# Kernel optimization log

Measured on AMD Instinct MI355X. Metric: run time of the kernel, lower is better.

The kernel has to match this reference:

```python
import jax, jax.numpy as jnp
import numpy as np

NUM_GRAPHS = 512

def _add_self_loops(edge_index, n):
    loop = jnp.arange(n, dtype=edge_index.dtype)
    row = jnp.concatenate([edge_index[0], loop])
    col = jnp.concatenate([edge_index[1], loop])
    return row, col

def _gcn_conv(x, W, b, row, col, norm, n):
    h = x @ W                              # [N, H] dense transform
    msgs = h[row] * norm[:, None]          # gather + normalize, [E+N, H]
    out = jax.ops.segment_sum(msgs, col, num_segments=n)
    return out + b

def setup_inputs() -> dict:
    key = jax.random.key(0)
    ks = jax.random.split(key, 10)
    N, E, F_IN, H, C = 50000, 800000, 128, 128, 16
    s = 1.0 / np.sqrt(H)
    return {
        "x": jax.random.normal(ks[0], (N, F_IN), dtype=jnp.float32),
        "edge_index": jax.random.randint(ks[1], (2, E), 0, N, dtype=jnp.int64),
        "batch": jnp.sort(jax.random.randint(ks[2], (N,), 0, NUM_GRAPHS, dtype=jnp.int64)),
        "W1": jax.random.normal(ks[3], (F_IN, H), dtype=jnp.float32) * s,
        "b1": jnp.zeros((H,), dtype=jnp.float32),
        "W2": jax.random.normal(ks[4], (H, H), dtype=jnp.float32) * s,
        "b2": jnp.zeros((H,), dtype=jnp.float32),
        "W3": jax.random.normal(ks[5], (H, H), dtype=jnp.float32) * s,
        "b3": jnp.zeros((H,), dtype=jnp.float32),
        "lin_W": jax.random.normal(ks[6], (H, C), dtype=jnp.float32) * s,
        "lin_b": jnp.zeros((C,), dtype=jnp.float32),
    }

def reference(x, edge_index, batch, W1, b1, W2, b2, W3, b3, lin_W, lin_b):
    n = x.shape[0]
    row, col = _add_self_loops(edge_index, n)
    # symmetric degree normalization (computed once, shared by all layers)
    deg = jax.ops.segment_sum(jnp.ones_like(col, dtype=x.dtype), col, num_segments=n)
    dinv = jnp.where(deg > 0, jax.lax.rsqrt(deg), 0.0)
    norm = dinv[row] * dinv[col]           # [E+N]

    h = jax.nn.relu(_gcn_conv(x, W1, b1, row, col, norm, n))
    h = jax.nn.relu(_gcn_conv(h, W2, b2, row, col, norm, n))
    h = _gcn_conv(h, W3, b3, row, col, norm, n)

    # global mean pool over graphs in the batch
    pooled = jax.ops.segment_sum(h, batch, num_segments=NUM_GRAPHS)
    cnt = jax.ops.segment_sum(jnp.ones((n,), dtype=h.dtype), batch, num_segments=NUM_GRAPHS)
    pooled = pooled / jnp.maximum(cnt, 1.0)[:, None]

    # dropout is identity in eval mode
    return pooled @ lin_W + lin_b          # [NUM_GRAPHS, C]
```

## Files before the change

kernel.cpp:

```cpp
#include <hip/hip_runtime.h>
#include <hip/hip_bf16.h>

#define FEAT 128
#define NGRAPH 512
#define NCLS 16

typedef __attribute__((ext_vector_type(8))) short bf16x8;
typedef __attribute__((ext_vector_type(4))) float f32x4;


__device__ inline unsigned short f2bf(float f) {
    __hip_bfloat16 h = __float2bfloat16(f);
    return *(unsigned short*)&h;
}
__device__ inline float bf2f(unsigned short u) {
    return __uint_as_float((unsigned int)u << 16);
}
__device__ inline void unpk2(unsigned int u, float& lo, float& hi) {
    lo = __uint_as_float(u << 16);
    hi = __uint_as_float(u & 0xffff0000u);
}


__global__ void k_hist(const int* __restrict__ col, int* __restrict__ hist, int E) {
    int i = blockIdx.x * blockDim.x + threadIdx.x;
    if (i < E) atomicAdd(&hist[col[i]], 1);
}

__global__ void k_dinv(const int* __restrict__ hist, float* __restrict__ dinv, int N) {
    int i = blockIdx.x * blockDim.x + threadIdx.x;
    if (i < N) dinv[i] = rsqrtf((float)(hist[i] + 1));
}

__global__ void k_scanA(const int* __restrict__ hist, int* __restrict__ partial, int N) {
    __shared__ int s[256];
    int i = blockIdx.x * 256 + threadIdx.x;
    s[threadIdx.x] = (i < N) ? hist[i] : 0;
    __syncthreads();
    for (int off = 128; off > 0; off >>= 1) {
        if (threadIdx.x < off) s[threadIdx.x] += s[threadIdx.x + off];
        __syncthreads();
    }
    if (threadIdx.x == 0) partial[blockIdx.x] = s[0];
}

__global__ void k_scanB(int* __restrict__ partial, int nb) {
    __shared__ int s[256];
    int t = threadIdx.x;
    int orig = (t < nb) ? partial[t] : 0;
    s[t] = orig;
    __syncthreads();
    for (int off = 1; off < 256; off <<= 1) {
        int v = (t >= off) ? s[t - off] : 0;
        __syncthreads();
        s[t] += v;
        __syncthreads();
    }
    if (t < nb) partial[t] = s[t] - orig;
}

__global__ void k_scanC(const int* __restrict__ hist, const int* __restrict__ partial,
                        int* __restrict__ start, int* __restrict__ cur, int N) {
    __shared__ int s[256];
    int t = threadIdx.x;
    int i = blockIdx.x * 256 + t;
    int orig = (i < N) ? hist[i] : 0;
    s[t] = orig;
    __syncthreads();
    for (int off = 1; off < 256; off <<= 1) {
        int v = (t >= off) ? s[t - off] : 0;
        __syncthreads();
        s[t] += v;
        __syncthreads();
    }
    if (i < N) {
        int ex = s[t] - orig + partial[blockIdx.x];
        start[i] = ex;
        cur[i] = ex;
    }
}

__global__ void k_fill(const int* __restrict__ row, const int* __restrict__ col,
                       int* __restrict__ cur, int* __restrict__ csr_row, int E) {
    int i = blockIdx.x * blockDim.x + threadIdx.x;
    if (i >= E) return;
    int r = row[i], c = col[i];
    int pos = atomicAdd(&cur[c], 1);
    csr_row[pos] = r;
}


__global__ void k_wsplit(const float* __restrict__ W1, const float* __restrict__ W2,
                         const float* __restrict__ W3,
                         bf16x8* __restrict__ whi, bf16x8* __restrict__ wlo) {
    int tid = blockIdx.x * 256 + threadIdx.x;
    int layer = tid >> 11;
    int r = tid & 2047;
    int kt = r >> 9, cb = (r >> 6) & 7, lane = r & 63;
    const float* W = (layer == 0) ? W1 : (layer == 1) ? W2 : W3;
    bf16x8 hi, lo;
    #pragma unroll
    for (int j = 0; j < 8; ++j) {
        float w = W[(size_t)(kt * 32 + (lane >> 4) * 8 + j) * FEAT + cb * 16 + (lane & 15)];
        unsigned short hb = f2bf(w);
        hi[j] = (short)hb;
        lo[j] = (short)f2bf(w - bf2f(hb));
    }
    size_t idx = (size_t)layer * 2048 + (kt * 8 + cb) * 64 + lane;
    whi[idx] = hi;
    wlo[idx] = lo;
}


__global__ __launch_bounds__(256) void k_gemm(const float* __restrict__ A,
                                              const bf16x8* __restrict__ Whi,
                                              const bf16x8* __restrict__ Wlo,
                                              const float* __restrict__ dinv,
                                              unsigned short* __restrict__ tbf, int M) {
    int tid = threadIdx.x;
    int wave = tid >> 6, lane = tid & 63;
    int m0 = blockIdx.x * 64 + wave * 16;
    int aclamp = min(m0 + (lane & 15), M - 1);
    int kgrp = lane >> 4;

    f32x4 acc[8];
    #pragma unroll
    for (int c = 0; c < 8; ++c) acc[c] = (f32x4){0.f, 0.f, 0.f, 0.f};

    #pragma unroll
    for (int kt = 0; kt < 4; ++kt) {
        const float* ap = A + (size_t)aclamp * FEAT + kt * 32 + kgrp * 8;
        float av[8];
        *(float4*)&av[0] = *(const float4*)ap;
        *(float4*)&av[4] = *(const float4*)(ap + 4);
        bf16x8 ahi, alo;
        #pragma unroll
        for (int j = 0; j < 8; ++j) {
            unsigned short hb = f2bf(av[j]);
            ahi[j] = (short)hb;
            alo[j] = (short)f2bf(av[j] - bf2f(hb));
        }
        #pragma unroll
        for (int cb = 0; cb < 8; ++cb) {
            bf16x8 bh = Whi[(kt * 8 + cb) * 64 + lane];
            bf16x8 bl = Wlo[(kt * 8 + cb) * 64 + lane];
            acc[cb] = __builtin_amdgcn_mfma_f32_16x16x32_bf16(ahi, bh, acc[cb], 0, 0, 0);
            acc[cb] = __builtin_amdgcn_mfma_f32_16x16x32_bf16(alo, bh, acc[cb], 0, 0, 0);
            acc[cb] = __builtin_amdgcn_mfma_f32_16x16x32_bf16(ahi, bl, acc[cb], 0, 0, 0);
        }
    }

    int rbase = m0 + (lane >> 4) * 4;
    int colb = lane & 15;
    #pragma unroll
    for (int r = 0; r < 4; ++r) {
        int gr = rbase + r;
        if (gr < M) {
            float dv = dinv[gr];
            #pragma unroll
            for (int cb = 0; cb < 8; ++cb)
                tbf[(size_t)gr * FEAT + cb * 16 + colb] = f2bf(acc[cb][r] * dv);
        }
    }
}


__global__ __launch_bounds__(256) void k_agg(const uint2* __restrict__ tbf,
                                             const int* __restrict__ csr_row,
                                             const int* __restrict__ start,
                                             const int* __restrict__ endp,
                                             const float* __restrict__ dinv,
                                             const float* __restrict__ bias,
                                             float* __restrict__ h, int N, int do_relu) {
    int t = threadIdx.x;
    int v = blockIdx.x * 8 + (t >> 5);
    if (v >= N) return;
    int lane = t & 31;

    float a0, a1, a2, a3;
    {
        uint2 sv = tbf[(size_t)v * 32 + lane];
        unpk2(sv.x, a0, a1); unpk2(sv.y, a2, a3);
    }

    int s = start[v], e = endp[v];
    int p = s;
    for (; p + 4 <= e; p += 4) {
        int r0 = csr_row[p], r1 = csr_row[p + 1], r2 = csr_row[p + 2], r3 = csr_row[p + 3];
        uint2 g0 = tbf[(size_t)r0 * 32 + lane];
        uint2 g1 = tbf[(size_t)r1 * 32 + lane];
        uint2 g2 = tbf[(size_t)r2 * 32 + lane];
        uint2 g3 = tbf[(size_t)r3 * 32 + lane];
        float f0, f1, f2, f3;
        unpk2(g0.x, f0, f1); unpk2(g0.y, f2, f3);
        a0 += f0; a1 += f1; a2 += f2; a3 += f3;
        unpk2(g1.x, f0, f1); unpk2(g1.y, f2, f3);
        a0 += f0; a1 += f1; a2 += f2; a3 += f3;
        unpk2(g2.x, f0, f1); unpk2(g2.y, f2, f3);
        a0 += f0; a1 += f1; a2 += f2; a3 += f3;
        unpk2(g3.x, f0, f1); unpk2(g3.y, f2, f3);
        a0 += f0; a1 += f1; a2 += f2; a3 += f3;
    }
    for (; p < e; ++p) {
        int r = csr_row[p];
        uint2 g = tbf[(size_t)r * 32 + lane];
        float f0, f1, f2, f3;
        unpk2(g.x, f0, f1); unpk2(g.y, f2, f3);
        a0 += f0; a1 += f1; a2 += f2; a3 += f3;
    }

    float dv = dinv[v];
    float4 b4 = *(const float4*)&bias[lane * 4];
    a0 = fmaf(a0, dv, b4.x); a1 = fmaf(a1, dv, b4.y);
    a2 = fmaf(a2, dv, b4.z); a3 = fmaf(a3, dv, b4.w);
    if (do_relu) {
        a0 = fmaxf(a0, 0.f); a1 = fmaxf(a1, 0.f);
        a2 = fmaxf(a2, 0.f); a3 = fmaxf(a3, 0.f);
    }
    *(float4*)&h[(size_t)v * FEAT + lane * 4] = make_float4(a0, a1, a2, a3);
}


__global__ void k_gcnt(const int* __restrict__ batch, int* __restrict__ gcnt, int N) {
    int v = blockIdx.x * blockDim.x + threadIdx.x;
    if (v < N) atomicAdd(&gcnt[batch[v]], 1);
}

__global__ void k_goff(const int* __restrict__ gcnt, int* __restrict__ goff,
                       float* __restrict__ cntf) {
    __shared__ int s[NGRAPH];
    int t = threadIdx.x;
    int v = gcnt[t];
    s[t] = v;
    __syncthreads();
    for (int off = 1; off < NGRAPH; off <<= 1) {
        int u = (t >= off) ? s[t - off] : 0;
        __syncthreads();
        s[t] += u;
        __syncthreads();
    }
    goff[t] = s[t] - v;
    cntf[t] = (float)v;
}

__global__ __launch_bounds__(128) void k_pool(const float* __restrict__ h,
                                              const int* __restrict__ goff,
                                              const int* __restrict__ gcnt,
                                              float* __restrict__ pooled) {
    int g = blockIdx.x, t = threadIdx.x;
    int s = goff[g], n = gcnt[g];
    float acc = 0.f;
    for (int i = 0; i < n; ++i) acc += h[(size_t)(s + i) * FEAT + t];
    pooled[g * FEAT + t] = acc / fmaxf((float)n, 1.f);
}

__global__ void k_final(const float* __restrict__ pooled,
                        const float* __restrict__ linW, const float* __restrict__ linb,
                        float* __restrict__ out) {
    int idx = blockIdx.x * blockDim.x + threadIdx.x;
    if (idx >= NGRAPH * NCLS) return;
    int g = idx >> 4, c = idx & 15;
    float acc = 0.f;
    #pragma unroll 8
    for (int jj = 0; jj < FEAT; ++jj)
        acc = fmaf(pooled[g * FEAT + jj], linW[jj * NCLS + c], acc);
    out[idx] = acc + linb[c];
}


extern "C" void kernel_launch(void* const* d_in, const int* in_sizes, int n_in,
                              void* d_out, int out_size, void* d_ws, size_t ws_size,
                              hipStream_t stream) {
    const float* x    = (const float*)d_in[0];
    const int*   ei   = (const int*)d_in[1];
    const int*   batch= (const int*)d_in[2];
    const float* W1   = (const float*)d_in[3];
    const float* b1   = (const float*)d_in[4];
    const float* W2   = (const float*)d_in[5];
    const float* b2   = (const float*)d_in[6];
    const float* W3   = (const float*)d_in[7];
    const float* b3   = (const float*)d_in[8];
    const float* linW = (const float*)d_in[9];
    const float* linb = (const float*)d_in[10];
    float* out = (float*)d_out;

    const int N = in_sizes[0] / FEAT;
    const int E = in_sizes[1] / 2;
    const int* row = ei;
    const int* col = ei + E;

    char* p = (char*)d_ws;
    auto alloc = [&](size_t bytes) { void* r = (void*)p; p += (bytes + 255) & ~(size_t)255; return r; };
    int*   hist    = (int*)  alloc((size_t)N * 4);
    int*   start   = (int*)  alloc((size_t)N * 4);
    int*   cur     = (int*)  alloc((size_t)N * 4);
    float* dinv    = (float*)alloc((size_t)N * 4);
    int*   csr_row = (int*)  alloc((size_t)E * 4);
    int*   partial = (int*)  alloc(4096);
    unsigned short* tbf = (unsigned short*)alloc((size_t)N * FEAT * 2);
    float* h       = (float*)alloc((size_t)N * FEAT * 4);
    bf16x8* whi    = (bf16x8*)alloc(3 * 2048 * sizeof(bf16x8));
    bf16x8* wlo    = (bf16x8*)alloc(3 * 2048 * sizeof(bf16x8));
    float* pooled  = (float*)alloc((size_t)NGRAPH * FEAT * 4);
    float* cntf    = (float*)alloc((size_t)NGRAPH * 4);
    int*   gcnt    = (int*)  alloc((size_t)NGRAPH * 4);
    int*   goff    = (int*)  alloc((size_t)NGRAPH * 4);

    hipMemsetAsync(hist, 0, (size_t)N * 4, stream);
    hipMemsetAsync(gcnt, 0, (size_t)NGRAPH * 4, stream);

    const int nscan = (N + 255) / 256;

    k_hist  <<<(E + 255) / 256, 256, 0, stream>>>(col, hist, E);
    k_dinv  <<<nscan, 256, 0, stream>>>(hist, dinv, N);
    k_scanA <<<nscan, 256, 0, stream>>>(hist, partial, N);
    k_scanB <<<1, 256, 0, stream>>>(partial, nscan);
    k_scanC <<<nscan, 256, 0, stream>>>(hist, partial, start, cur, N);
    k_fill  <<<(E + 255) / 256, 256, 0, stream>>>(row, col, cur, csr_row, E);
    k_wsplit<<<24, 256, 0, stream>>>(W1, W2, W3, whi, wlo);
    k_gcnt  <<<nscan, 256, 0, stream>>>(batch, gcnt, N);
    k_goff  <<<1, NGRAPH, 0, stream>>>(gcnt, goff, cntf);

    const int gblk = (N + 63) / 64;
    const int ablk = (N + 7) / 8;

    k_gemm<<<gblk, 256, 0, stream>>>(x, whi,        wlo,        dinv, tbf, N);
    k_agg <<<ablk, 256, 0, stream>>>((const uint2*)tbf, csr_row, start, cur, dinv, b1, h, N, 1);
    k_gemm<<<gblk, 256, 0, stream>>>(h, whi + 2048, wlo + 2048, dinv, tbf, N);
    k_agg <<<ablk, 256, 0, stream>>>((const uint2*)tbf, csr_row, start, cur, dinv, b2, h, N, 1);
    k_gemm<<<gblk, 256, 0, stream>>>(h, whi + 4096, wlo + 4096, dinv, tbf, N);
    k_agg <<<ablk, 256, 0, stream>>>((const uint2*)tbf, csr_row, start, cur, dinv, b3, h, N, 0);

    k_pool <<<NGRAPH, 128, 0, stream>>>(h, goff, gcnt, pooled);
    k_final<<<(NGRAPH * NCLS + 255) / 256, 256, 0, stream>>>(pooled, linW, linb, out);
}
```

Before: 426.0 us.

## Store hidden activations and CSR neighbor indices in 16-bit formats

Result: no change. 423.2 us (-0.7%).

```diff
diff --git a/kernel.cpp b/kernel.cpp
--- a/kernel.cpp
+++ b/kernel.cpp
@@ -15,6 +15,9 @@
 }
 __device__ inline float bf2f(unsigned short u) {
     return __uint_as_float((unsigned int)u << 16);
+}
+__device__ inline unsigned int pk2(float a, float b) {
+    return (unsigned int)f2bf(a) | ((unsigned int)f2bf(b) << 16);
 }
 __device__ inline void unpk2(unsigned int u, float& lo, float& hi) {
     lo = __uint_as_float(u << 16);
@@ -81,12 +84,12 @@
 }
 
 __global__ void k_fill(const int* __restrict__ row, const int* __restrict__ col,
-                       int* __restrict__ cur, int* __restrict__ csr_row, int E) {
+                       int* __restrict__ cur, unsigned short* __restrict__ csr_row, int E) {
     int i = blockIdx.x * blockDim.x + threadIdx.x;
     if (i >= E) return;
     int r = row[i], c = col[i];
     int pos = atomicAdd(&cur[c], 1);
-    csr_row[pos] = r;
+    __builtin_nontemporal_store((unsigned short)r, &csr_row[pos]);
 }
 
 
@@ -112,11 +115,11 @@
 }
 
 
-__global__ __launch_bounds__(256) void k_gemm(const float* __restrict__ A,
-                                              const bf16x8* __restrict__ Whi,
-                                              const bf16x8* __restrict__ Wlo,
-                                              const float* __restrict__ dinv,
-                                              unsigned short* __restrict__ tbf, int M) {
+__global__ __launch_bounds__(256) void k_gemm_f32(const float* __restrict__ A,
+                                                  const bf16x8* __restrict__ Whi,
+                                                  const bf16x8* __restrict__ Wlo,
+                                                  const float* __restrict__ dinv,
+                                                  unsigned short* __restrict__ tbf, int M) {
     int tid = threadIdx.x;
     int wave = tid >> 6, lane = tid & 63;
     int m0 = blockIdx.x * 64 + wave * 16;
@@ -165,13 +168,57 @@
 }
 
 
+__global__ __launch_bounds__(256) void k_gemm_bf16(const unsigned short* __restrict__ Abf,
+                                                   const bf16x8* __restrict__ Whi,
+                                                   const bf16x8* __restrict__ Wlo,
+                                                   const float* __restrict__ dinv,
+                                                   unsigned short* __restrict__ tbf, int M) {
+    int tid = threadIdx.x;
+    int wave = tid >> 6, lane = tid & 63;
+    int m0 = blockIdx.x * 64 + wave * 16;
+    int aclamp = min(m0 + (lane & 15), M - 1);
+    int kgrp = lane >> 4;
+
+    f32x4 acc[8];
+    #pragma unroll
+    for (int c = 0; c < 8; ++c) acc[c] = (f32x4){0.f, 0.f, 0.f, 0.f};
+
+    #pragma unroll
+    for (int kt = 0; kt < 4; ++kt) {
+        bf16x8 ahi = *(const bf16x8*)(Abf + (size_t)aclamp * FEAT + kt * 32 + kgrp * 8);
+        #pragma unroll
+        for (int cb = 0; cb < 8; ++cb) {
+            bf16x8 bh = Whi[(kt * 8 + cb) * 64 + lane];
+            bf16x8 bl = Wlo[(kt * 8 + cb) * 64 + lane];
+            acc[cb] = __builtin_amdgcn_mfma_f32_16x16x32_bf16(ahi, bh, acc[cb], 0, 0, 0);
+            acc[cb] = __builtin_amdgcn_mfma_f32_16x16x32_bf16(ahi, bl, acc[cb], 0, 0, 0);
+        }
+    }
+
+    int rbase = m0 + (lane >> 4) * 4;
+    int colb = lane & 15;
+    #pragma unroll
+    for (int r = 0; r < 4; ++r) {
+        int gr = rbase + r;
+        if (gr < M) {
+            float dv = dinv[gr];
+            #pragma unroll
+            for (int cb = 0; cb < 8; ++cb)
+                tbf[(size_t)gr * FEAT + cb * 16 + colb] = f2bf(acc[cb][r] * dv);
+        }
+    }
+}
+
+
 __global__ __launch_bounds__(256) void k_agg(const uint2* __restrict__ tbf,
-                                             const int* __restrict__ csr_row,
+                                             const unsigned short* __restrict__ csr_row,
                                              const int* __restrict__ start,
                                              const int* __restrict__ endp,
                                              const float* __restrict__ dinv,
                                              const float* __restrict__ bias,
-                                             float* __restrict__ h, int N, int do_relu) {
+                                             float* __restrict__ hf,
+                                             uint2* __restrict__ hb,
+                                             int N, int mode) {
     int t = threadIdx.x;
     int v = blockIdx.x * 8 + (t >> 5);
     if (v >= N) return;
@@ -213,11 +260,16 @@
     float4 b4 = *(const float4*)&bias[lane * 4];
     a0 = fmaf(a0, dv, b4.x); a1 = fmaf(a1, dv, b4.y);
     a2 = fmaf(a2, dv, b4.z); a3 = fmaf(a3, dv, b4.w);
-    if (do_relu) {
+    if (mode) {
         a0 = fmaxf(a0, 0.f); a1 = fmaxf(a1, 0.f);
         a2 = fmaxf(a2, 0.f); a3 = fmaxf(a3, 0.f);
-    }
-    *(float4*)&h[(size_t)v * FEAT + lane * 4] = make_float4(a0, a1, a2, a3);
+        uint2 o;
+        o.x = pk2(a0, a1);
+        o.y = pk2(a2, a3);
+        hb[(size_t)v * 32 + lane] = o;
+    } else {
+        *(float4*)&hf[(size_t)v * FEAT + lane * 4] = make_float4(a0, a1, a2, a3);
+    }
 }
 
 
@@ -295,9 +347,10 @@
     int*   start   = (int*)  alloc((size_t)N * 4);
     int*   cur     = (int*)  alloc((size_t)N * 4);
     float* dinv    = (float*)alloc((size_t)N * 4);
-    int*   csr_row = (int*)  alloc((size_t)E * 4);
+    unsigned short* csr_row = (unsigned short*)alloc((size_t)E * 2);
     int*   partial = (int*)  alloc(4096);
     unsigned short* tbf = (unsigned short*)alloc((size_t)N * FEAT * 2);
+    unsigned short* hbb = (unsigned short*)alloc((size_t)N * FEAT * 2);
     float* h       = (float*)alloc((size_t)N * FEAT * 4);
     bf16x8* whi    = (bf16x8*)alloc(3 * 2048 * sizeof(bf16x8));
     bf16x8* wlo    = (bf16x8*)alloc(3 * 2048 * sizeof(bf16x8));
@@ -324,12 +377,15 @@
     const int gblk = (N + 63) / 64;
     const int ablk = (N + 7) / 8;
 
-    k_gemm<<<gblk, 256, 0, stream>>>(x, whi,        wlo,        dinv, tbf, N);
-    k_agg <<<ablk, 256, 0, stream>>>((const uint2*)tbf, csr_row, start, cur, dinv, b1, h, N, 1);
-    k_gemm<<<gblk, 256, 0, stream>>>(h, whi + 2048, wlo + 2048, dinv, tbf, N);
-    k_agg <<<ablk, 256, 0, stream>>>((const uint2*)tbf, csr_row, start, cur, dinv, b2, h, N, 1);
-    k_gemm<<<gblk, 256, 0, stream>>>(h, whi + 4096, wlo + 4096, dinv, tbf, N);
-    k_agg <<<ablk, 256, 0, stream>>>((const uint2*)tbf, csr_row, start, cur, dinv, b3, h, N, 0);
+    k_gemm_f32 <<<gblk, 256, 0, stream>>>(x, whi, wlo, dinv, tbf, N);
+    k_agg      <<<ablk, 256, 0, stream>>>((const uint2*)tbf, csr_row, start, cur, dinv, b1,
+                                          nullptr, (uint2*)hbb, N, 1);
+    k_gemm_bf16<<<gblk, 256, 0, stream>>>(hbb, whi + 2048, wlo + 2048, dinv, tbf, N);
+    k_agg      <<<ablk, 256, 0, stream>>>((const uint2*)tbf, csr_row, start, cur, dinv, b2,
+                                          nullptr, (uint2*)hbb, N, 1);
+    k_gemm_bf16<<<gblk, 256, 0, stream>>>(hbb, whi + 4096, wlo + 4096, dinv, tbf, N);
+    k_agg      <<<ablk, 256, 0, stream>>>((const uint2*)tbf, csr_row, start, cur, dinv, b3,
+                                          h, nullptr, N, 0);
 
     k_pool <<<NGRAPH, 128, 0, stream>>>(h, goff, gcnt, pooled);
     k_final<<<(NGRAPH * NCLS + 255) / 256, 256, 0, stream>>>(pooled, linW, linb, out);
```
